# Kernel tuning notes

Measured on AMD Instinct MI355X. Metric: run time of the kernel, lower is better.

## Reference

```python
import jax, jax.numpy as jnp
import numpy as np

N = 50000      # nodes
E = 800000     # edges (avg degree 16)
F_IN = 3       # dataset.num_node_features
H = 256        # hidden_channels
G = 64         # batch_size (num graphs)
OUT = 24       # lin_out output dim


def setup_inputs() -> dict:
    key = jax.random.key(0)
    ks = jax.random.split(key, 16)
    s = 0.05
    inp = {
        "x": jax.random.normal(ks[0], (N, F_IN), jnp.float32),
        "edge_index": jax.random.randint(ks[1], (2, E), 0, N, dtype=jnp.int32),
        "batch": jnp.sort(jax.random.randint(ks[2], (N,), 0, G, dtype=jnp.int32)),
        # layer 1 (F_IN -> H)
        "w_rel1": jax.random.normal(ks[3], (F_IN, H), jnp.float32) * s,
        "w_root1": jax.random.normal(ks[4], (F_IN, H), jnp.float32) * s,
        "b1": jnp.zeros((H,), jnp.float32),
        # layers 2..7 (H -> H), stacked
        "w_rel": jax.random.normal(ks[5], (6, H, H), jnp.float32) * s,
        "w_root": jax.random.normal(ks[6], (6, H, H), jnp.float32) * s,
        "b": jnp.zeros((6, H), jnp.float32),
        # output head
        "w_out": jax.random.normal(ks[7], (H, OUT), jnp.float32) * s,
        "b_out": jnp.zeros((OUT,), jnp.float32),
    }
    return inp


def reference(x, edge_index, batch, w_rel1, w_root1, b1, w_rel, w_root, b, w_out, b_out):
    src, dst = edge_index[0], edge_index[1]

    def conv(h, wr, wro, bb):
        # PyG GraphConv with add aggregation:
        # out_i = W_rel @ sum_{j -> i} h_j + b + W_root @ h_i
        agg = jax.ops.segment_sum(h[src], dst, num_segments=N)
        return agg @ wr + h @ wro + bb

    h = jax.nn.relu(conv(x, w_rel1, w_root1, b1))
    for i in range(6):
        h = jax.nn.relu(conv(h, w_rel[i], w_root[i], b[i]))

    # global_mean_pool over batch segment ids
    counts = jax.ops.segment_sum(jnp.ones((N,), h.dtype), batch, num_segments=G)
    pooled = jax.ops.segment_sum(h, batch, num_segments=G) / jnp.maximum(counts, 1.0)[:, None]

    # dropout is identity in eval mode
    return pooled @ w_out + b_out
```

## Files before the change

kernel.cpp:

```cpp
#include <hip/hip_runtime.h>

#define N_NODES 50000
#define MPAD 50048
#define N_EDGES 800000
#define H 256
#define K_CAT 512
#define G_BATCH 64
#define OUT_DIM 24

#define SCAN_BLK 256
#define NBLK ((N_NODES + SCAN_BLK - 1) / SCAN_BLK)

typedef __attribute__((ext_vector_type(8))) short short8;
typedef __attribute__((ext_vector_type(4))) float float4v;

__device__ __forceinline__ float bf2f(unsigned short u) {
    return __uint_as_float(((unsigned)u) << 16);
}
__device__ __forceinline__ unsigned short f2bf(float f) {
    unsigned x = __float_as_uint(f);
    unsigned r = (x + 0x7FFFu + ((x >> 16) & 1u)) >> 16;
    return (unsigned short)r;
}

__device__ __forceinline__ void async_copy16(void* lds, const void* g) {
    __builtin_amdgcn_global_load_lds(
        (const __attribute__((address_space(1))) unsigned int*)g,
        (__attribute__((address_space(3))) unsigned int*)lds, 16, 0, 0);
}



__global__ void histo_kernel(const int* __restrict__ dst, int* __restrict__ deg,
                             int* __restrict__ epos) {
    int e = blockIdx.x * blockDim.x + threadIdx.x;
    if (e < N_EDGES) epos[e] = atomicAdd(&deg[dst[e]], 1);
}

__global__ void scan_block(const int* __restrict__ deg, int* __restrict__ rowptr,
                           int* __restrict__ blockSums) {
    __shared__ int s[SCAN_BLK];
    int idx = blockIdx.x * SCAN_BLK + threadIdx.x;
    int v = (idx < N_NODES) ? deg[idx] : 0;
    s[threadIdx.x] = v;
    __syncthreads();
    for (int off = 1; off < SCAN_BLK; off <<= 1) {
        int t = (threadIdx.x >= off) ? s[threadIdx.x - off] : 0;
        __syncthreads();
        s[threadIdx.x] += t;
        __syncthreads();
    }
    if (idx < N_NODES) rowptr[idx] = s[threadIdx.x] - v;
    if (threadIdx.x == SCAN_BLK - 1) blockSums[blockIdx.x] = s[threadIdx.x];
}

__global__ void scan_finish(int* __restrict__ rowptr, const int* __restrict__ blockSums) {
    __shared__ int s[SCAN_BLK];
    int t = threadIdx.x;
    int v = (t < NBLK) ? blockSums[t] : 0;
    s[t] = v;
    __syncthreads();
    for (int off = 1; off < SCAN_BLK; off <<= 1) {
        int tv = (t >= off) ? s[t - off] : 0;
        __syncthreads();
        s[t] += tv;
        __syncthreads();
    }
    int prefix = (blockIdx.x > 0) ? s[blockIdx.x - 1] : 0;
    int idx = blockIdx.x * SCAN_BLK + t;
    if (idx < N_NODES) rowptr[idx] += prefix;
    if (blockIdx.x == 0 && t == 0) rowptr[N_NODES] = s[NBLK - 1];
}

__global__ void fill_csr(const int* __restrict__ src, const int* __restrict__ dst,
                         const int* __restrict__ rowptr, const int* __restrict__ epos,
                         int* __restrict__ csr_src) {
    int e = blockIdx.x * blockDim.x + threadIdx.x;
    if (e >= N_EDGES) return;
    csr_src[rowptr[dst[e]] + epos[e]] = src[e];
}


__global__ void prep_weights(const float* __restrict__ w_rel, const float* __restrict__ w_root,
                             unsigned short* __restrict__ WcatT) {
    int idx = blockIdx.x * blockDim.x + threadIdx.x;
    if (idx >= 6 * K_CAT * H) return;
    int n = idx & (H - 1);
    int k = (idx >> 8) & (K_CAT - 1);
    int l = idx >> 17;
    float v;
    if (k < H) {
        int f = (k & 0xC0) | ((k & 3) << 4) | ((k >> 2) & 15);
        v = w_rel[(size_t)l * H * H + f * H + n];
    } else {
        int b = k - H;
        int f = (b & 0xC0) | ((b & 3) << 4) | ((b >> 2) & 15);
        v = w_root[(size_t)l * H * H + f * H + n];
    }
    WcatT[(size_t)l * H * K_CAT + (size_t)n * K_CAT + k] = f2bf(v);
}


__global__ void layer1_kernel(const float* __restrict__ x, const int* __restrict__ rowptr,
                              const int* __restrict__ csr_src,
                              const float* __restrict__ wr, const float* __restrict__ wro,
                              const float* __restrict__ bias,
                              unsigned char* __restrict__ h8, float* __restrict__ hscale) {
    __shared__ unsigned char tmp[H];
    __shared__ float sagg[3];
    int n = blockIdx.x;
    int f = threadIdx.x;
    int lane = f & 63;

    if (f < 64) {
        int beg = rowptr[n], end = rowptr[n + 1];
        float a0 = 0.f, a1 = 0.f, a2 = 0.f;
        for (int i = beg + lane; i < end; i += 64) {
            int s = csr_src[i];
            a0 += x[s * 3 + 0];
            a1 += x[s * 3 + 1];
            a2 += x[s * 3 + 2];
        }
#pragma unroll
        for (int off = 1; off < 64; off <<= 1) {
            a0 += __shfl_xor(a0, off, 64);
            a1 += __shfl_xor(a1, off, 64);
            a2 += __shfl_xor(a2, off, 64);
        }
        if (lane == 0) { sagg[0] = a0; sagg[1] = a1; sagg[2] = a2; }
    }
    __syncthreads();

    float a0 = sagg[0], a1 = sagg[1], a2 = sagg[2];
    float x0 = x[n * 3 + 0], x1 = x[n * 3 + 1], x2 = x[n * 3 + 2];
    float v = bias[f];
    v += a0 * wr[0 * H + f] + a1 * wr[1 * H + f] + a2 * wr[2 * H + f];
    v += x0 * wro[0 * H + f] + x1 * wro[1 * H + f] + x2 * wro[2 * H + f];
    v = fmaxf(v, 0.f);
    float m = v;
#pragma unroll
    for (int off = 1; off < 64; off <<= 1) m = fmaxf(m, __shfl_xor(m, off, 64));
    float inv = m > 0.f ? 255.f / m : 0.f;
    tmp[(f & 0xC0) | ((f & 15) << 2) | ((f >> 4) & 3)] = (unsigned char)(v * inv + 0.5f);
    if ((f & 63) == 0) hscale[n * 4 + (f >> 6)] = m * (1.f / 255.f);
    __syncthreads();
    if (f < 64) *(unsigned*)(h8 + (size_t)n * H + f * 4) = *(const unsigned*)(tmp + f * 4);
}


__global__ __launch_bounds__(256) void aggH(unsigned short* __restrict__ aggcat,
                                            const unsigned char* __restrict__ h8,
                                            const float* __restrict__ hscale,
                                            const int* __restrict__ rowptr,
                                            const int* __restrict__ csr_src) {
    int gtid = blockIdx.x * blockDim.x + threadIdx.x;
    int node = gtid >> 6;
    if (node >= N_NODES) return;
    int lane = threadIdx.x & 63;
    int sub = lane >> 4;
    int fl = lane & 15;
    int g = fl >> 2;
    int beg = rowptr[node], end = rowptr[node + 1];

    if (beg >= end) {
        if (sub == 0) {
            uint4 z = make_uint4(0, 0, 0, 0);
            unsigned short* o = aggcat + (size_t)node * H + fl * 16;
            *(uint4*)o = z;
            *(uint4*)(o + 8) = z;
        }
        return;
    }

    float acc[16] = {};
    const unsigned char* base = h8 + fl * 16;
    int last = end - 1;

    int i0 = beg + sub;
    int i1 = beg + 4 + sub;
    int i2 = beg + 8 + sub;
    int i3 = beg + 12 + sub;
    int s0 = csr_src[i0 < end ? i0 : last];
    int s1 = csr_src[i1 < end ? i1 : last];
    int s2 = csr_src[i2 < end ? i2 : last];
    int s3 = csr_src[i3 < end ? i3 : last];
    float sc0 = (i0 < end) ? hscale[s0 * 4 + g] : 0.f;
    float sc1 = (i1 < end) ? hscale[s1 * 4 + g] : 0.f;
    uint4 q0 = *(const uint4*)(base + (size_t)s0 * H);
    uint4 q1 = *(const uint4*)(base + (size_t)s1 * H);

    for (int i = beg; i < end; i += 4) {
        int i4 = i + 16 + sub;
        int s4 = csr_src[i4 < end ? i4 : last];
        int ic = i + 8 + sub;
        float sc2 = (ic < end) ? hscale[s2 * 4 + g] : 0.f;
        uint4 q2 = *(const uint4*)(base + (size_t)s2 * H);

        float sc = sc0;
        acc[0]  = fmaf((float)(q0.x & 0xffu), sc, acc[0]);
        acc[1]  = fmaf((float)((q0.x >> 8) & 0xffu), sc, acc[1]);
        acc[2]  = fmaf((float)((q0.x >> 16) & 0xffu), sc, acc[2]);
        acc[3]  = fmaf((float)(q0.x >> 24), sc, acc[3]);
        acc[4]  = fmaf((float)(q0.y & 0xffu), sc, acc[4]);
        acc[5]  = fmaf((float)((q0.y >> 8) & 0xffu), sc, acc[5]);
        acc[6]  = fmaf((float)((q0.y >> 16) & 0xffu), sc, acc[6]);
        acc[7]  = fmaf((float)(q0.y >> 24), sc, acc[7]);
        acc[8]  = fmaf((float)(q0.z & 0xffu), sc, acc[8]);
        acc[9]  = fmaf((float)((q0.z >> 8) & 0xffu), sc, acc[9]);
        acc[10] = fmaf((float)((q0.z >> 16) & 0xffu), sc, acc[10]);
        acc[11] = fmaf((float)(q0.z >> 24), sc, acc[11]);
        acc[12] = fmaf((float)(q0.w & 0xffu), sc, acc[12]);
        acc[13] = fmaf((float)((q0.w >> 8) & 0xffu), sc, acc[13]);
        acc[14] = fmaf((float)((q0.w >> 16) & 0xffu), sc, acc[14]);
        acc[15] = fmaf((float)(q0.w >> 24), sc, acc[15]);

        q0 = q1; q1 = q2;
        sc0 = sc1; sc1 = sc2;
        s2 = s3; s3 = s4;
    }

#pragma unroll
    for (int j = 0; j < 16; j++) {
        acc[j] += __shfl_xor(acc[j], 16, 64);
        acc[j] += __shfl_xor(acc[j], 32, 64);
    }

    if (sub == 0) {
        unsigned short* o = aggcat + (size_t)node * H + fl * 16;
        uint4 p0, p1;
        p0.x = (unsigned)f2bf(acc[0])  | ((unsigned)f2bf(acc[1]) << 16);
        p0.y = (unsigned)f2bf(acc[2])  | ((unsigned)f2bf(acc[3]) << 16);
        p0.z = (unsigned)f2bf(acc[4])  | ((unsigned)f2bf(acc[5]) << 16);
        p0.w = (unsigned)f2bf(acc[6])  | ((unsigned)f2bf(acc[7]) << 16);
        p1.x = (unsigned)f2bf(acc[8])  | ((unsigned)f2bf(acc[9]) << 16);
        p1.y = (unsigned)f2bf(acc[10]) | ((unsigned)f2bf(acc[11]) << 16);
        p1.z = (unsigned)f2bf(acc[12]) | ((unsigned)f2bf(acc[13]) << 16);
        p1.w = (unsigned)f2bf(acc[14]) | ((unsigned)f2bf(acc[15]) << 16);
        *(uint4*)o = p0;
        *(uint4*)(o + 8) = p1;
    }
}


#define GBM 64
#define GBN 128
#define GBK 64

__global__ __launch_bounds__(256) void gemm_mfma(
    const unsigned short* __restrict__ aggcat, const unsigned char* __restrict__ h8in,
    const float* __restrict__ hscin, const unsigned short* __restrict__ WcatT,
    const float* __restrict__ bias,
    unsigned char* __restrict__ h8out, float* __restrict__ hscout) {
    __shared__ unsigned short sA[GBM][GBK];
    __shared__ unsigned short sB[GBN][GBK];

    const int tid = threadIdx.x;
    const int wave = tid >> 6;
    const int lane = tid & 63;
    const int quad = lane >> 4;
    const int l16 = lane & 15;
    const int wm0 = (wave & 1) * 32;
    const int wn0 = (wave >> 1) * 64;
    const int m0 = blockIdx.x * GBM;
    const int n0 = blockIdx.y * GBN;

    const int rowoff = lane >> 3;
    const int schunk = ((lane & 7) ^ rowoff) * 8;
    const unsigned short* Aagg[2];
    const unsigned short* Bsrc[4];
#pragma unroll
    for (int j = 0; j < 2; j++) {
        int q = wave * 2 + j;
        Aagg[j] = aggcat + (size_t)(m0 + q * 8 + rowoff) * H + schunk;
    }
#pragma unroll
    for (int j = 0; j < 4; j++) {
        int q = wave * 4 + j;
        Bsrc[j] = WcatT + (size_t)(n0 + q * 8 + rowoff) * K_CAT + schunk;
    }

    const int r_row = wave * 16 + (lane >> 3);
    const int r_bc = lane & 7;
    const unsigned char* r_src0 = h8in + (size_t)(m0 + r_row) * H + r_bc * 8;
    const unsigned char* r_src1 = r_src0 + 8 * H;
    const float* sc0p = hscin + (size_t)(m0 + r_row) * 4;
    const float* sc1p = sc0p + 32;
    const int ldsoff = wave * 2048 + (lane >> 3) * 128 + ((lane & 7) ^ (lane >> 3)) * 16;
    unsigned short* ldst0 = (unsigned short*)((char*)sA + ldsoff);
    unsigned short* ldst1 = (unsigned short*)((char*)sA + ldsoff + 1024);

    const int sw = l16 & 7;
    const int ca0 = (quad ^ sw) * 8;
    const int ca1 = ((4 + quad) ^ sw) * 8;

    float4v acc[2][4] = {};

#define COMPUTE()                                                            \
    {                                                                        \
        short8 a[2][2], b[4][2];                                             \
        _Pragma("unroll") for (int i = 0; i < 2; i++) {                      \
            const unsigned short* ra = &sA[wm0 + i * 16 + l16][0];           \
            a[i][0] = *(const short8*)(ra + ca0);                            \
            a[i][1] = *(const short8*)(ra + ca1);                            \
        }                                                                    \
        _Pragma("unroll") for (int i = 0; i < 4; i++) {                      \
            const unsigned short* rb = &sB[wn0 + i * 16 + l16][0];           \
            b[i][0] = *(const short8*)(rb + ca0);                            \
            b[i][1] = *(const short8*)(rb + ca1);                            \
        }                                                                    \
        _Pragma("unroll") for (int sub = 0; sub < 2; sub++)                  \
            _Pragma("unroll") for (int mi = 0; mi < 2; mi++)                 \
                _Pragma("unroll") for (int ni = 0; ni < 4; ni++)             \
                    acc[mi][ni] = __builtin_amdgcn_mfma_f32_16x16x32_bf16(   \
                        a[mi][sub], b[ni][sub], acc[mi][ni], 0, 0, 0);       \
    }

    for (int kk = 0; kk < 256; kk += GBK) {
#pragma unroll
        for (int j = 0; j < 2; j++)
            async_copy16((char*)sA + (wave * 2 + j) * 1024, Aagg[j] + kk);
#pragma unroll
        for (int j = 0; j < 4; j++)
            async_copy16((char*)sB + (wave * 4 + j) * 1024, Bsrc[j] + kk);
        __syncthreads();
        COMPUTE();
        __syncthreads();
    }

#pragma unroll
    for (int kb = 0; kb < 4; kb++) {
        const int kk = 256 + kb * GBK;
#pragma unroll
        for (int j = 0; j < 4; j++)
            async_copy16((char*)sB + (wave * 4 + j) * 1024, Bsrc[j] + kk);
        {
            uint2 q0 = *(const uint2*)(r_src0 + kb * GBK);
            uint2 q1 = *(const uint2*)(r_src1 + kb * GBK);
            float s0 = sc0p[kb];
            float s1 = sc1p[kb];
            uint4 p0, p1;
            p0.x = (unsigned)f2bf((float)(q0.x & 0xffu) * s0)
                 | ((unsigned)f2bf((float)((q0.x >> 8) & 0xffu) * s0) << 16);
            p0.y = (unsigned)f2bf((float)((q0.x >> 16) & 0xffu) * s0)
                 | ((unsigned)f2bf((float)(q0.x >> 24) * s0) << 16);
            p0.z = (unsigned)f2bf((float)(q0.y & 0xffu) * s0)
                 | ((unsigned)f2bf((float)((q0.y >> 8) & 0xffu) * s0) << 16);
            p0.w = (unsigned)f2bf((float)((q0.y >> 16) & 0xffu) * s0)
                 | ((unsigned)f2bf((float)(q0.y >> 24) * s0) << 16);
            p1.x = (unsigned)f2bf((float)(q1.x & 0xffu) * s1)
                 | ((unsigned)f2bf((float)((q1.x >> 8) & 0xffu) * s1) << 16);
            p1.y = (unsigned)f2bf((float)((q1.x >> 16) & 0xffu) * s1)
                 | ((unsigned)f2bf((float)(q1.x >> 24) * s1) << 16);
            p1.z = (unsigned)f2bf((float)(q1.y & 0xffu) * s1)
                 | ((unsigned)f2bf((float)((q1.y >> 8) & 0xffu) * s1) << 16);
            p1.w = (unsigned)f2bf((float)((q1.y >> 16) & 0xffu) * s1)
                 | ((unsigned)f2bf((float)(q1.y >> 24) * s1) << 16);
            *(uint4*)ldst0 = p0;
            *(uint4*)ldst1 = p1;
        }
        __syncthreads();
        COMPUTE();
        __syncthreads();
    }
#undef COMPUTE

    const int hb = n0 + wn0 + l16 * 4;
    const int gsc = (n0 + wn0) >> 6;
    float bcol[4];
#pragma unroll
    for (int ni = 0; ni < 4; ni++) bcol[ni] = bias[n0 + wn0 + ni * 16 + l16];

#pragma unroll
    for (int mi = 0; mi < 2; mi++) {
        int rowb = m0 + wm0 + mi * 16 + quad * 4;
#pragma unroll
        for (int r = 0; r < 4; r++) {
            int row = rowb + r;
            float v0 = fmaxf(acc[mi][0][r] + bcol[0], 0.f);
            float v1 = fmaxf(acc[mi][1][r] + bcol[1], 0.f);
            float v2 = fmaxf(acc[mi][2][r] + bcol[2], 0.f);
            float v3 = fmaxf(acc[mi][3][r] + bcol[3], 0.f);
            float m = fmaxf(fmaxf(v0, v1), fmaxf(v2, v3));
            m = fmaxf(m, __shfl_xor(m, 1, 64));
            m = fmaxf(m, __shfl_xor(m, 2, 64));
            m = fmaxf(m, __shfl_xor(m, 4, 64));
            m = fmaxf(m, __shfl_xor(m, 8, 64));
            float inv = m > 0.f ? 255.f / m : 0.f;
            unsigned p = (unsigned)(v0 * inv + 0.5f)
                       | ((unsigned)(v1 * inv + 0.5f) << 8)
                       | ((unsigned)(v2 * inv + 0.5f) << 16)
                       | ((unsigned)(v3 * inv + 0.5f) << 24);
            *(unsigned*)(h8out + (size_t)row * H + hb) = p;
            if (l16 == 0) hscout[row * 4 + gsc] = m * (1.f / 255.f);
        }
    }
}


__device__ __forceinline__ int lowerBound(const int* __restrict__ batch, int val) {
    int lo = 0, hi = N_NODES;
    while (lo < hi) {
        int mid = (lo + hi) >> 1;
        if (batch[mid] < val) lo = mid + 1; else hi = mid;
    }
    return lo;
}

__global__ void pool_partial(const unsigned char* __restrict__ h8,
                             const float* __restrict__ hscale,
                             const int* __restrict__ batch, float* __restrict__ pooled) {
    int g = blockIdx.x;
    int seg = blockIdx.y;
    int bpos = threadIdx.x;
    int grp = bpos >> 6;
    int start = lowerBound(batch, g);
    int end = lowerBound(batch, g + 1);
    int len = end - start;
    int s0 = start + (int)((long long)len * seg / 8);
    int s1 = start + (int)((long long)len * (seg + 1) / 8);
    float sum = 0.f;
    for (int n = s0; n < s1; ++n)
        sum += (float)h8[(size_t)n * H + bpos] * hscale[n * 4 + grp];
    if (s1 > s0)
        atomicAdd(&pooled[g * H + bpos], sum);
}

__global__ void head_kernel(const float* __restrict__ pooled, const int* __restrict__ batch,
                            const float* __restrict__ w_out, const float* __restrict__ b_out,
                            float* __restrict__ out) {
    int g = blockIdx.x;
    int o = threadIdx.x;
    int start = lowerBound(batch, g);
    int end = lowerBound(batch, g + 1);
    float cnt = fmaxf((float)(end - start), 1.f);
    float sum = 0.f;
    for (int bpos = 0; bpos < H; ++bpos) {
        int f = (bpos & 0xC0) | ((bpos & 3) << 4) | ((bpos >> 2) & 15);
        sum += pooled[g * H + bpos] * w_out[f * OUT_DIM + o];
    }
    out[g * OUT_DIM + o] = b_out[o] + sum / cnt;
}


extern "C" void kernel_launch(void* const* d_in, const int* in_sizes, int n_in,
                              void* d_out, int out_size, void* d_ws, size_t ws_size,
                              hipStream_t stream) {
    const float* x      = (const float*)d_in[0];
    const int*   ei     = (const int*)d_in[1];
    const int*   batch  = (const int*)d_in[2];
    const float* w_rel1 = (const float*)d_in[3];
    const float* w_root1= (const float*)d_in[4];
    const float* b1     = (const float*)d_in[5];
    const float* w_rel  = (const float*)d_in[6];
    const float* w_root = (const float*)d_in[7];
    const float* b      = (const float*)d_in[8];
    const float* w_out  = (const float*)d_in[9];
    const float* b_out  = (const float*)d_in[10];
    float* out = (float*)d_out;

    const int* src = ei;
    const int* dst = ei + N_EDGES;

    unsigned short* aggcat = (unsigned short*)d_ws;
    unsigned short* WcatT  = aggcat + (size_t)MPAD * H;
    unsigned char* h8a = (unsigned char*)(WcatT + (size_t)6 * H * K_CAT);
    unsigned char* h8b = h8a + (size_t)MPAD * H;
    float* hsa     = (float*)(h8b + (size_t)MPAD * H);
    float* hsb     = hsa + (size_t)MPAD * 4;
    float* pooled  = hsb + (size_t)MPAD * 4;
    int* rowptr    = (int*)(pooled + G_BATCH * H);
    int* degcur    = rowptr + (N_NODES + 1);
    int* blockSums = degcur + N_NODES;
    int* csr_src   = blockSums + SCAN_BLK;
    int* epos      = csr_src + N_EDGES;

    hipMemsetAsync(degcur, 0, N_NODES * sizeof(int), stream);
    histo_kernel<<<(N_EDGES + 255) / 256, 256, 0, stream>>>(dst, degcur, epos);
    scan_block<<<NBLK, SCAN_BLK, 0, stream>>>(degcur, rowptr, blockSums);
    scan_finish<<<NBLK, SCAN_BLK, 0, stream>>>(rowptr, blockSums);
    fill_csr<<<(N_EDGES + 255) / 256, 256, 0, stream>>>(src, dst, rowptr, epos, csr_src);

    prep_weights<<<(6 * K_CAT * H + 255) / 256, 256, 0, stream>>>(w_rel, w_root, WcatT);

    layer1_kernel<<<N_NODES, H, 0, stream>>>(x, rowptr, csr_src, w_rel1, w_root1, b1,
                                             h8a, hsa);

    unsigned char* h8c = h8a; float* hsc = hsa;
    unsigned char* h8n = h8b; float* hsn = hsb;
    for (int l = 0; l < 6; ++l) {
        aggH<<<(N_NODES * 64 + 255) / 256, 256, 0, stream>>>(aggcat, h8c, hsc, rowptr, csr_src);
        dim3 grid(MPAD / GBM, H / GBN);
        gemm_mfma<<<grid, 256, 0, stream>>>(aggcat, h8c, hsc,
                                            WcatT + (size_t)l * H * K_CAT,
                                            b + (size_t)l * H, h8n, hsn);
        unsigned char* t8 = h8c; h8c = h8n; h8n = t8;
        float* tf = hsc; hsc = hsn; hsn = tf;
    }

    hipMemsetAsync(pooled, 0, G_BATCH * H * sizeof(float), stream);
    pool_partial<<<dim3(G_BATCH, 8), 256, 0, stream>>>(h8c, hsc, batch, pooled);
    head_kernel<<<G_BATCH, OUT_DIM, 0, stream>>>(pooled, batch, w_out, b_out, out);
}
```

Before: 629.6 us.

## Process layer-1 nodes one per wavefront with register quantize and bpermute transpose

Layer 1 now maps one 64-lane wavefront to each node, four nodes per block, instead of a 256-thread block per node. Each lane computes four features and takes per-group maxima with shuffles. The byte interleave is done through ds_bpermute rather than shared memory, which removes both __syncthreads and the shared buffers. This cuts block-launch and sync overhead and removes the three idle wavefronts per block during gather, at the cost of more serial work per lane.

```diff
diff --git a/kernel.cpp b/kernel.cpp
--- a/kernel.cpp
+++ b/kernel.cpp
@@ -101,50 +101,71 @@
 }
 
 
-__global__ void layer1_kernel(const float* __restrict__ x, const int* __restrict__ rowptr,
-                              const int* __restrict__ csr_src,
-                              const float* __restrict__ wr, const float* __restrict__ wro,
-                              const float* __restrict__ bias,
-                              unsigned char* __restrict__ h8, float* __restrict__ hscale) {
-    __shared__ unsigned char tmp[H];
-    __shared__ float sagg[3];
-    int n = blockIdx.x;
-    int f = threadIdx.x;
-    int lane = f & 63;
-
-    if (f < 64) {
-        int beg = rowptr[n], end = rowptr[n + 1];
-        float a0 = 0.f, a1 = 0.f, a2 = 0.f;
-        for (int i = beg + lane; i < end; i += 64) {
-            int s = csr_src[i];
-            a0 += x[s * 3 + 0];
-            a1 += x[s * 3 + 1];
-            a2 += x[s * 3 + 2];
-        }
-#pragma unroll
-        for (int off = 1; off < 64; off <<= 1) {
-            a0 += __shfl_xor(a0, off, 64);
-            a1 += __shfl_xor(a1, off, 64);
-            a2 += __shfl_xor(a2, off, 64);
-        }
-        if (lane == 0) { sagg[0] = a0; sagg[1] = a1; sagg[2] = a2; }
-    }
-    __syncthreads();
-
-    float a0 = sagg[0], a1 = sagg[1], a2 = sagg[2];
-    float x0 = x[n * 3 + 0], x1 = x[n * 3 + 1], x2 = x[n * 3 + 2];
-    float v = bias[f];
-    v += a0 * wr[0 * H + f] + a1 * wr[1 * H + f] + a2 * wr[2 * H + f];
-    v += x0 * wro[0 * H + f] + x1 * wro[1 * H + f] + x2 * wro[2 * H + f];
-    v = fmaxf(v, 0.f);
-    float m = v;
-#pragma unroll
-    for (int off = 1; off < 64; off <<= 1) m = fmaxf(m, __shfl_xor(m, off, 64));
-    float inv = m > 0.f ? 255.f / m : 0.f;
-    tmp[(f & 0xC0) | ((f & 15) << 2) | ((f >> 4) & 3)] = (unsigned char)(v * inv + 0.5f);
-    if ((f & 63) == 0) hscale[n * 4 + (f >> 6)] = m * (1.f / 255.f);
-    __syncthreads();
-    if (f < 64) *(unsigned*)(h8 + (size_t)n * H + f * 4) = *(const unsigned*)(tmp + f * 4);
+__global__ __launch_bounds__(256) void layer1_kernel(
+    const float* __restrict__ x, const int* __restrict__ rowptr,
+    const int* __restrict__ csr_src,
+    const float* __restrict__ wr, const float* __restrict__ wro,
+    const float* __restrict__ bias,
+    unsigned char* __restrict__ h8, float* __restrict__ hscale) {
+    int gtid = blockIdx.x * blockDim.x + threadIdx.x;
+    int node = gtid >> 6;
+    if (node >= N_NODES) return;
+    int lane = threadIdx.x & 63;
+
+    int beg = rowptr[node], end = rowptr[node + 1];
+    float a0 = 0.f, a1 = 0.f, a2 = 0.f;
+    for (int i = beg + lane; i < end; i += 64) {
+        int s = csr_src[i];
+        a0 += x[s * 3 + 0];
+        a1 += x[s * 3 + 1];
+        a2 += x[s * 3 + 2];
+    }
+#pragma unroll
+    for (int off = 1; off < 64; off <<= 1) {
+        a0 += __shfl_xor(a0, off, 64);
+        a1 += __shfl_xor(a1, off, 64);
+        a2 += __shfl_xor(a2, off, 64);
+    }
+
+    float x0 = x[node * 3 + 0], x1 = x[node * 3 + 1], x2 = x[node * 3 + 2];
+
+    float v[4], mm[4];
+#pragma unroll
+    for (int g = 0; g < 4; g++) {
+        int f = g * 64 + lane;
+        float t = bias[f];
+        t += a0 * wr[0 * H + f] + a1 * wr[1 * H + f] + a2 * wr[2 * H + f];
+        t += x0 * wro[0 * H + f] + x1 * wro[1 * H + f] + x2 * wro[2 * H + f];
+        t = fmaxf(t, 0.f);
+        v[g] = t;
+        float m = t;
+#pragma unroll
+        for (int off = 1; off < 64; off <<= 1) m = fmaxf(m, __shfl_xor(m, off, 64));
+        mm[g] = m;
+    }
+
+    unsigned qp = 0;
+#pragma unroll
+    for (int g = 0; g < 4; g++) {
+        float inv = mm[g] > 0.f ? 255.f / mm[g] : 0.f;
+        qp |= ((unsigned)(v[g] * inv + 0.5f)) << (8 * g);
+    }
+
+    int grp = lane >> 4;
+    unsigned w = 0;
+#pragma unroll
+    for (int j = 0; j < 4; j++) {
+        int sj = (j << 4) | (lane & 15);
+        unsigned r = (unsigned)__builtin_amdgcn_ds_bpermute(sj << 2, (int)qp);
+        w |= ((r >> (8 * grp)) & 0xffu) << (8 * j);
+    }
+    *(unsigned*)(h8 + (size_t)node * H + lane * 4) = w;
+
+    if (lane == 0) {
+        float4 s4 = make_float4(mm[0] * (1.f / 255.f), mm[1] * (1.f / 255.f),
+                                mm[2] * (1.f / 255.f), mm[3] * (1.f / 255.f));
+        *(float4*)(&hscale[node * 4]) = s4;
+    }
 }
 
 
@@ -482,8 +503,8 @@
 
     prep_weights<<<(6 * K_CAT * H + 255) / 256, 256, 0, stream>>>(w_rel, w_root, WcatT);
 
-    layer1_kernel<<<N_NODES, H, 0, stream>>>(x, rowptr, csr_src, w_rel1, w_root1, b1,
-                                             h8a, hsa);
+    layer1_kernel<<<(N_NODES * 64 + 255) / 256, 256, 0, stream>>>(
+        x, rowptr, csr_src, w_rel1, w_root1, b1, h8a, hsa);
 
     unsigned char* h8c = h8a; float* hsc = hsa;
     unsigned char* h8n = h8b; float* hsn = hsb;
```

Measured after the change: 609.8 us. 1.03x faster.
